# Optimization experiments

Measured on AMD Instinct MI355X. Metric: run time of the kernel, lower is better.

Reference implementation:

```python
import jax, jax.numpy as jnp
import numpy as np

N0, N1, N2, N3, B = 120000, 20000, 6000, 1600, 64
E1, E2, E3 = 480000, 144000, 38400
KS = 5  # kernel size per dim; K = 125 total


def spline_basis(pseudo, ks=KS):
    # open B-spline basis, degree 1, over [0,1]^3 (torch_spline_conv semantics)
    p = pseudo * (ks - 1)                       # (E,3)
    lo = jnp.clip(jnp.floor(p), 0.0, ks - 2.0)  # (E,3)
    f = p - lo                                  # fractional part
    bits = jnp.array([[(s >> d) & 1 for d in range(3)] for s in range(8)],
                     dtype=jnp.float32)         # (8,3) corner offsets
    w = jnp.where(bits[None] > 0, f[:, None, :], 1.0 - f[:, None, :])  # (E,8,3)
    basis = w[..., 0] * w[..., 1] * w[..., 2]   # (E,8)
    strides = jnp.array([1.0, ks, ks * ks], dtype=jnp.float32)
    kidx = ((lo[:, None, :] + bits[None]) * strides).sum(-1).astype(jnp.int32)  # (E,8)
    return basis, kidx


def spline_conv(x, edge_index, pseudo, W, root, bias, num_nodes):
    src, dst = edge_index[0], edge_index[1]
    basis, kidx = spline_basis(pseudo)                   # (E,8), (E,8)
    XW = jnp.einsum('ni,kio->nko', x, W)                 # (N,K,out)
    taps = XW[src[:, None], kidx]                        # (E,8,out) gather
    msg = (taps * basis[..., None]).sum(axis=1)          # (E,out)
    agg = jax.ops.segment_sum(msg, dst, num_segments=num_nodes)
    deg = jax.ops.segment_sum(jnp.ones_like(dst, jnp.float32), dst,
                              num_segments=num_nodes)
    agg = agg / jnp.maximum(deg, 1.0)[:, None]           # mean aggregation
    return agg + x @ root + bias


def seg_max(x, seg, n):
    v = jax.ops.segment_max(x, seg, num_segments=n)
    return jnp.where(jnp.isfinite(v), v, 0.0)  # empty voxels -> 0


def setup_inputs() -> dict:
    key = jax.random.key(0)
    ks = jax.random.split(key, 24)
    return {
        'x0': jax.random.uniform(ks[0], (N0, 1), jnp.float32),
        'cluster0': jax.random.randint(ks[1], (N0,), 0, N1),
        'edge1': jax.random.randint(ks[2], (2, E1), 0, N1),
        'pseudo1': jax.random.uniform(ks[3], (E1, 3), jnp.float32),
        'W1': jax.random.normal(ks[4], (125, 1, 64), jnp.float32) * 0.1,
        'root1': jax.random.normal(ks[5], (1, 64), jnp.float32) * 0.1,
        'b1': jnp.zeros((64,), jnp.float32),
        'cluster1': jax.random.randint(ks[6], (N1,), 0, N2),
        'edge2': jax.random.randint(ks[7], (2, E2), 0, N2),
        'pseudo2': jax.random.uniform(ks[8], (E2, 3), jnp.float32),
        'W2': jax.random.normal(ks[9], (125, 64, 64), jnp.float32) * 0.05,
        'root2': jax.random.normal(ks[10], (64, 64), jnp.float32) * 0.05,
        'b2': jnp.zeros((64,), jnp.float32),
        'cluster2': jax.random.randint(ks[11], (N2,), 0, N3),
        'edge3': jax.random.randint(ks[12], (2, E3), 0, N3),
        'pseudo3': jax.random.uniform(ks[13], (E3, 3), jnp.float32),
        'W3': jax.random.normal(ks[14], (125, 64, 128), jnp.float32) * 0.05,
        'root3': jax.random.normal(ks[15], (64, 128), jnp.float32) * 0.05,
        'b3': jnp.zeros((128,), jnp.float32),
        'cluster3': jax.random.randint(ks[16], (N3,), 0, B * 8),
        'fc1_w': jax.random.normal(ks[17], (1024, 256), jnp.float32) * 0.03,
        'fc1_b': jnp.zeros((256,), jnp.float32),
        'fc2_w': jax.random.normal(ks[18], (256, 10), jnp.float32) * 0.06,
        'fc2_b': jnp.zeros((10,), jnp.float32),
    }


def reference(x0, cluster0, edge1, pseudo1, W1, root1, b1,
              cluster1, edge2, pseudo2, W2, root2, b2,
              cluster2, edge3, pseudo3, W3, root3, b3,
              cluster3, fc1_w, fc1_b, fc2_w, fc2_b):
    x = seg_max(x0, cluster0, N1)                       # sparse voxel max pool 1
    x = jax.nn.elu(spline_conv(x, edge1, pseudo1, W1, root1, b1, N1))
    x = seg_max(x, cluster1, N2)                        # pool 2
    x = jax.nn.elu(spline_conv(x, edge2, pseudo2, W2, root2, b2, N2))
    x = seg_max(x, cluster2, N3)                        # pool 3
    x = jax.nn.elu(spline_conv(x, edge3, pseudo3, W3, root3, b3, N3))
    x = seg_max(x, cluster3, B * 8)                     # dense 2x2x2 voxel pool
    x = x.reshape(B, 8 * 128)
    x = jax.nn.elu(x @ fc1_w + fc1_b)
    x = x @ fc2_w + fc2_b
    return jax.nn.log_softmax(x, axis=1)
```

## Files before the change

### kernel.cpp

```cpp
#include <hip/hip_runtime.h>
#include <hip/hip_bf16.h>
#include <hip/hip_fp16.h>
#include <math.h>

#define N0c 120000
#define N1c 20000
#define N2c 6000
#define N3c 1600
#define E1c 480000
#define E2c 144000
#define E3c 38400

#define HB1 256
#define HB2 480
#define HB3 160
#define WCVB 125
#define SS0B  469

typedef __attribute__((ext_vector_type(8))) short short8;
typedef __attribute__((ext_vector_type(4))) float f32x4;

__device__ __forceinline__ float eluf(float x) {
    return x > 0.0f ? x : expm1f(x);
}

__device__ __forceinline__ unsigned f2sort(float f) {
    unsigned u = __float_as_uint(f);
    return (u & 0x80000000u) ? ~u : (u | 0x80000000u);
}
__device__ __forceinline__ float sort2f(unsigned u) {
    unsigned bits = (u & 0x80000000u) ? (u & 0x7FFFFFFFu) : ~u;
    return __uint_as_float(bits);
}
__device__ __forceinline__ unsigned short f2bf(float v) {
    unsigned u = __float_as_uint(v);
    unsigned r = (u + 0x7FFFu + ((u >> 16) & 1u)) >> 16;
    return (unsigned short)r;
}
__device__ __forceinline__ unsigned short f2h(float v) {
    return __half_as_ushort(__float2half(v));
}
__device__ __forceinline__ float h2f(unsigned short u) {
    return __half2float(__ushort_as_half(u));
}

__global__ __launch_bounds__(256) void hist_all(
    const int* __restrict__ edge1, const int* __restrict__ edge2,
    const int* __restrict__ edge3,
    const float* __restrict__ pseudo2, const float* __restrict__ pseudo3,
    const float* __restrict__ W2, const float* __restrict__ W3,
    const float* __restrict__ x0, const int* __restrict__ cluster0,
    int* __restrict__ blockCnt1, int* __restrict__ binTot1,
    int* __restrict__ blockCnt2, int* __restrict__ binTot2, int* __restrict__ cntD2,
    int* __restrict__ blockCnt3, int* __restrict__ binTot3, int* __restrict__ cntD3,
    unsigned short* __restrict__ W2t, unsigned short* __restrict__ W3t,
    unsigned* __restrict__ xm1)
{
    __shared__ float smf[64 * 129];
    int* h = (int*)smf;
    int b = blockIdx.x, t = threadIdx.x;
    if (b < HB1) {
        for (int i = t; i < 1250; i += 256) h[i] = 0;
        __syncthreads();
        for (int e = b * 256 + t; e < E1c; e += HB1 * 256)
            atomicAdd(&h[edge1[E1c + e] >> 4], 1);
        __syncthreads();
        for (int i = t; i < 1250; i += 256) {
            int v = h[i];
            blockCnt1[i * HB1 + b] = v;
            if (v) atomicAdd(&binTot1[i], v);
        }
    } else if (b < HB1 + HB2 + HB3) {
        bool is2 = b < HB1 + HB2;
        int rb = is2 ? (b - HB1) : (b - HB1 - HB2);
        int nblk = is2 ? HB2 : HB3;
        int E = is2 ? E2c : E3c;
        const int* edge = is2 ? edge2 : edge3;
        const float* pseudo = is2 ? pseudo2 : pseudo3;
        int* blockCnt = is2 ? blockCnt2 : blockCnt3;
        int* binTot = is2 ? binTot2 : binTot3;
        int* dstCnt = is2 ? cntD2 : cntD3;
        int nb = is2 ? HB2 : HB3;
        if (t < 64) h[t] = 0;
        __syncthreads();
        for (int e = rb * 256 + t; e < E; e += nblk * 256) {
            int c = 0, mul = 1;
            #pragma unroll
            for (int d = 0; d < 3; d++) {
                float p = pseudo[e * 3 + d] * 4.0f;
                float l = fminf(fmaxf(floorf(p), 0.0f), 3.0f);
                c += (int)l * mul;
                mul <<= 2;
            }
            atomicAdd(&h[c], 1);
            atomicAdd(&dstCnt[edge[E + e]], 1);
        }
        __syncthreads();
        if (t < 64) {
            int v = h[t];
            blockCnt[t * nb + rb] = v;
            if (v) atomicAdd(&binTot[t], v);
        }
    } else if (b < HB1 + HB2 + HB3 + WCVB) {
        int k = b - (HB1 + HB2 + HB3);
        for (int idx = t; idx < 4096; idx += 256) {
            int n = idx & 63, ic = idx >> 6;
            smf[ic * 65 + n] = W2[((size_t)k * 64 + ic) * 64 + n];
        }
        __syncthreads();
        for (int idx = t; idx < 4096; idx += 256) {
            int ic = idx & 63, n = idx >> 6;
            W2t[((size_t)k * 64 + n) * 64 + ic] = f2bf(smf[ic * 65 + n]);
        }
    } else if (b < HB1 + HB2 + HB3 + 2 * WCVB) {
        int k = b - (HB1 + HB2 + HB3 + WCVB);
        for (int idx = t; idx < 8192; idx += 256) {
            int n = idx & 127, ic = idx >> 7;
            smf[ic * 129 + n] = W3[((size_t)k * 64 + ic) * 128 + n];
        }
        __syncthreads();
        for (int idx = t; idx < 8192; idx += 256) {
            int ic = idx & 63, n = idx >> 6;
            W3t[((size_t)k * 128 + n) * 64 + ic] = f2bf(smf[ic * 129 + n]);
        }
    } else {
        int idx = (b - (HB1 + HB2 + HB3 + 2 * WCVB)) * 256 + t;
        if (idx < N0c)
            atomicMax(&xm1[cluster0[idx]], f2sort(x0[idx]));
    }
}

__global__ __launch_bounds__(256) void plan_tot(
    const int* __restrict__ binTot1, int* __restrict__ start1,
    const int* __restrict__ binTot2, int* __restrict__ binCnt2,
    int* __restrict__ binStart2, int* __restrict__ blkPrefix2,
    int* __restrict__ chunkBin2, int* __restrict__ chunkOff2,
    const int* __restrict__ binTot3, int* __restrict__ binCnt3,
    int* __restrict__ binStart3, int* __restrict__ blkPrefix3,
    int* __restrict__ chunkBin3, int* __restrict__ chunkOff3,
    const int* __restrict__ cntD2, int* __restrict__ dstStart2,
    const int* __restrict__ cntD3, int* __restrict__ dstStart3)
{
    __shared__ int ps[256];
    __shared__ int ps64[64];
    int t = threadIdx.x;

    {
        int loc[5];
        int s = 0;
        #pragma unroll
        for (int i = 0; i < 5; i++) {
            int bin = t * 5 + i;
            int v = (bin < 1250) ? binTot1[bin] : 0;
            loc[i] = v;
            s += v;
        }
        ps[t] = s;
        __syncthreads();
        for (int ofs = 1; ofs < 256; ofs <<= 1) {
            int add = (t >= ofs) ? ps[t - ofs] : 0;
            __syncthreads();
            ps[t] += add;
            __syncthreads();
        }
        int run = (t == 0) ? 0 : ps[t - 1];
        #pragma unroll
        for (int i = 0; i < 5; i++) {
            int bin = t * 5 + i;
            if (bin < 1250) {
                start1[bin] = run;
                run += loc[i];
            }
        }
        if (t == 255) start1[1250] = run;
    }
    __syncthreads();

    if (t < 64) {
        int v = binTot2[t];
        binCnt2[t] = v;
        ps64[t] = v;
    }
    __syncthreads();
    if (t == 0) {
        int s2 = 0, p = 0;
        for (int c = 0; c < 64; c++) {
            int v = ps64[c];
            binStart2[c] = s2;
            blkPrefix2[c] = p;
            s2 += v;
            p += (v + 63) >> 6;
        }
        binStart2[64] = s2;
        blkPrefix2[64] = p;
    }
    __syncthreads();
    if (t < 64) {
        int nch = (binCnt2[t] + 63) >> 6;
        int base = blkPrefix2[t];
        for (int j = 0; j < nch; j++) {
            chunkBin2[base + j] = t;
            chunkOff2[base + j] = j;
        }
    }
    __syncthreads();

    if (t < 64) {
        int v = binTot3[t];
        binCnt3[t] = v;
        ps64[t] = v;
    }
    __syncthreads();
    if (t == 0) {
        int s3 = 0, p = 0;
        for (int c = 0; c < 64; c++) {
            int v = ps64[c];
            binStart3[c] = s3;
            blkPrefix3[c] = p;
            s3 += v;
            p += (v + 63) >> 6;
        }
        binStart3[64] = s3;
        blkPrefix3[64] = p;
    }
    __syncthreads();
    if (t < 64) {
        int nch = (binCnt3[t] + 63) >> 6;
        int base = blkPrefix3[t];
        for (int j = 0; j < nch; j++) {
            chunkBin3[base + j] = t;
            chunkOff3[base + j] = j;
        }
    }
    __syncthreads();

    {
        int locd[24];
        int sd = 0;
        #pragma unroll
        for (int i = 0; i < 24; i++) {
            int bin = t * 24 + i;
            int vv = (bin < N2c) ? cntD2[bin] : 0;
            locd[i] = vv;
            sd += vv;
        }
        ps[t] = sd;
        __syncthreads();
        for (int ofs = 1; ofs < 256; ofs <<= 1) {
            int add = (t >= ofs) ? ps[t - ofs] : 0;
            __syncthreads();
            ps[t] += add;
            __syncthreads();
        }
        int rund = (t == 0) ? 0 : ps[t - 1];
        #pragma unroll
        for (int i = 0; i < 24; i++) {
            int bin = t * 24 + i;
            if (bin < N2c) { dstStart2[bin] = rund; rund += locd[i]; }
        }
        if (t == 255) dstStart2[N2c] = ps[255];
    }
    __syncthreads();

    {
        int locd[7];
        int sd = 0;
        #pragma unroll
        for (int i = 0; i < 7; i++) {
            int bin = t * 7 + i;
            int vv = (bin < N3c) ? cntD3[bin] : 0;
            locd[i] = vv;
            sd += vv;
        }
        ps[t] = sd;
        __syncthreads();
        for (int ofs = 1; ofs < 256; ofs <<= 1) {
            int add = (t >= ofs) ? ps[t - ofs] : 0;
            __syncthreads();
            ps[t] += add;
            __syncthreads();
        }
        int rund = (t == 0) ? 0 : ps[t - 1];
        #pragma unroll
        for (int i = 0; i < 7; i++) {
            int bin = t * 7 + i;
            if (bin < N3c) { dstStart3[bin] = rund; rund += locd[i]; }
        }
        if (t == 255) dstStart3[N3c] = ps[255];
    }
}

__global__ __launch_bounds__(256) void off_all(
    const int* __restrict__ blockCnt1, const int* __restrict__ start1,
    int* __restrict__ blockOff1,
    const int* __restrict__ blockCnt2, const int* __restrict__ binStart2,
    int* __restrict__ blockOff2,
    const int* __restrict__ blockCnt3, const int* __restrict__ binStart3,
    int* __restrict__ blockOff3)
{
    int wid = (blockIdx.x * 256 + threadIdx.x) >> 6;
    int lane = threadIdx.x & 63;
    if (wid >= 1250 + 64 + 64) return;
    const int* c;
    int* o;
    int run, width;
    if (wid < 1250) {
        c = blockCnt1 + (size_t)wid * HB1;
        o = blockOff1 + (size_t)wid * HB1;
        run = start1[wid];
        width = HB1;
    } else if (wid < 1250 + 64) {
        int bin = wid - 1250;
        c = blockCnt2 + (size_t)bin * HB2;
        o = blockOff2 + (size_t)bin * HB2;
        run = binStart2[bin];
        width = HB2;
    } else {
        int bin = wid - 1314;
        c = blockCnt3 + (size_t)bin * HB3;
        o = blockOff3 + (size_t)bin * HB3;
        run = binStart3[bin];
        width = HB3;
    }
    for (int base = 0; base < width; base += 64) {
        int b = base + lane;
        int v = (b < width) ? c[b] : 0;
        int inc = v;
        #pragma unroll
        for (int ofs = 1; ofs < 64; ofs <<= 1) {
            int u = __shfl_up(inc, ofs);
            if (lane >= ofs) inc += u;
        }
        if (b < width) o[b] = run + inc - v;
        run += __shfl(inc, 63);
    }
}

__global__ __launch_bounds__(256) void scatter_all(
    const int* __restrict__ edge1, const float* __restrict__ pseudo1,
    const int* __restrict__ edge2, const float* __restrict__ pseudo2,
    const int* __restrict__ edge3, const float* __restrict__ pseudo3,
    const int* __restrict__ blockOff1,
    const int* __restrict__ blockOff2, const int* __restrict__ blockOff3,
    int4* __restrict__ rec1, int4* __restrict__ rec2, int4* __restrict__ rec3,
    unsigned* __restrict__ xm1,
    const int* __restrict__ dstStart2, const int* __restrict__ dstStart3,
    int* __restrict__ curD2, int* __restrict__ curD3,
    int* __restrict__ posList2, int* __restrict__ posList3)
{
    __shared__ int cur[1250];
    int b = blockIdx.x, t = threadIdx.x;
    if (b < HB1) {
        for (int i = t; i < 1250; i += 256) cur[i] = blockOff1[(size_t)i * HB1 + b];
        __syncthreads();
        for (int e = b * 256 + t; e < E1c; e += HB1 * 256) {
            int src = edge1[e], dst = edge1[E1c + e];
            float f[3];
            int kbase = 0, mul5 = 1;
            #pragma unroll
            for (int d = 0; d < 3; d++) {
                float pp = pseudo1[e * 3 + d] * 4.0f;
                float l = fminf(fmaxf(floorf(pp), 0.0f), 3.0f);
                f[d] = pp - l;
                kbase += (int)l * mul5;
                mul5 *= 5;
            }
            int p = atomicAdd(&cur[dst >> 4], 1);
            rec1[p] = make_int4(src | ((dst & 15) << 16) | (kbase << 20),
                                __float_as_int(f[0]), __float_as_int(f[1]),
                                __float_as_int(f[2]));
        }
    } else if (b < HB1 + HB2 + HB3) {
        bool is2 = b < HB1 + HB2;
        int rb = is2 ? (b - HB1) : (b - HB1 - HB2);
        int nblk = is2 ? HB2 : HB3;
        int E = is2 ? E2c : E3c;
        const int* edge = is2 ? edge2 : edge3;
        const float* pseudo = is2 ? pseudo2 : pseudo3;
        const int* blockOff = is2 ? blockOff2 : blockOff3;
        int4* rec = is2 ? rec2 : rec3;
        const int* dstStart = is2 ? dstStart2 : dstStart3;
        int* curD = is2 ? curD2 : curD3;
        int* posList = is2 ? posList2 : posList3;
        int nb = is2 ? HB2 : HB3;
        if (t < 64) cur[t] = blockOff[(size_t)t * nb + rb];
        __syncthreads();
        for (int e = rb * 256 + t; e < E; e += nblk * 256) {
            int src = edge[e], dst = edge[E + e];
            float f[3];
            int c = 0, mul = 1;
            #pragma unroll
            for (int d = 0; d < 3; d++) {
                float pp = pseudo[e * 3 + d] * 4.0f;
                float l = fminf(fmaxf(floorf(pp), 0.0f), 3.0f);
                f[d] = pp - l;
                c += (int)l * mul;
                mul <<= 2;
            }
            int p = atomicAdd(&cur[c], 1);
            rec[p] = make_int4(src | (dst << 16),
                               __float_as_int(f[0]), __float_as_int(f[1]),
                               __float_as_int(f[2]));
            int qd = dstStart[dst] + atomicAdd(&curD[dst], 1);
            posList[qd] = p;
        }
    } else {
        int idx = (b - (HB1 + HB2 + HB3)) * 256 + t;
        if (idx < N1c) {
            float f = sort2f(xm1[idx]);
            unsigned bb = __float_as_uint(f);
            if ((bb & 0x7F800000u) == 0x7F800000u) f = 0.0f;
            ((float*)xm1)[idx] = f;
        }
    }
}

__global__ __launch_bounds__(256) void conv1_block(
    const int4* __restrict__ rec, const float* __restrict__ x,
    const int* __restrict__ start,
    const float* __restrict__ W, const float* __restrict__ root,
    const float* __restrict__ bias, const int* __restrict__ cl,
    unsigned* __restrict__ xmOut) {
    __shared__ float T[16][128];
    __shared__ float Wl[8000];
    __shared__ int degL[16];
    int b = blockIdx.x;
    int t = threadIdx.x;
    for (int j = t; j < 2048; j += 256) ((float*)T)[j] = 0.0f;
    for (int j = t; j < 8000; j += 256) Wl[j] = W[j];
    if (t < 16) degL[t] = 0;
    __syncthreads();
    int s0 = start[b], s1 = start[b + 1];
    for (int i = s0 + t; i < s1; i += 256) {
        int4 r = rec[i];
        int src = r.x & 0xFFFF;
        int ln = (r.x >> 16) & 15;
        int kbase = r.x >> 20;
        float f0 = __int_as_float(r.y);
        float f1 = __int_as_float(r.z);
        float f2 = __int_as_float(r.w);
        float xv = x[src];
        #pragma unroll
        for (int s = 0; s < 8; s++) {
            int b0 = s & 1, b1 = (s >> 1) & 1, b2 = (s >> 2) & 1;
            float w0 = b0 ? f0 : 1.0f - f0;
            float w1 = b1 ? f1 : 1.0f - f1;
            float w2 = b2 ? f2 : 1.0f - f2;
            int k = kbase + b0 + 5 * b1 + 25 * b2;
            atomicAdd(&T[ln][k], xv * w0 * w1 * w2);
        }
        atomicAdd(&degL[ln], 1);
    }
    __syncthreads();
    int w = t >> 6, lane = t & 63;
    float acc[4] = {0.0f, 0.0f, 0.0f, 0.0f};
    #pragma unroll 5
    for (int k = 0; k < 125; k++) {
        float wv = Wl[(k << 6) + lane];
        #pragma unroll
        for (int j = 0; j < 4; j++)
            acc[j] = fmaf(T[w + 4 * j][k], wv, acc[j]);
    }
    int v0 = b << 4;
    #pragma unroll
    for (int j = 0; j < 4; j++) {
        int ln = w + 4 * j;
        int v = v0 + ln;
        float d = fmaxf((float)degL[ln], 1.0f);
        float val = eluf(acc[j] / d + x[v] * root[lane] + bias[lane]);
        atomicMax(&xmOut[((size_t)cl[v] << 6) + lane], f2sort(val));
    }
}

__global__ void decode_cvt(unsigned* __restrict__ buf,
                           unsigned short* __restrict__ xb, int total) {
    int idx = blockIdx.x * blockDim.x + threadIdx.x;
    if (idx >= total) return;
    float f = sort2f(buf[idx]);
    unsigned b = __float_as_uint(f);
    if ((b & 0x7F800000u) == 0x7F800000u) f = 0.0f;
    ((float*)buf)[idx] = f;
    xb[idx] = f2bf(f);
}

template<int COUT>
__global__ __launch_bounds__(256) void spline_mfma(
    const int4* __restrict__ recs,
    const unsigned short* __restrict__ Wt,
    const unsigned short* __restrict__ xb,
    const int* __restrict__ binStart,
    const int* __restrict__ binCnt,
    const int* __restrict__ blkPrefix,
    const int* __restrict__ chunkBin,
    const int* __restrict__ chunkOff,
    unsigned short* __restrict__ msg)
{
    __shared__ float basisS[4][8][64];
    __shared__ int srcS[4][64];

    int w = threadIdx.x >> 6, lane = threadIdx.x & 63;
    int c = blockIdx.x * 4 + w;
    if (c >= blkPrefix[64]) return;
    int bin = chunkBin[c];
    int chunk = chunkOff[c];
    int cnt = binCnt[bin];

    {
        int pos = chunk * 64 + lane;
        bool act = pos < cnt;
        int4 r = act ? recs[binStart[bin] + pos] : make_int4(0, 0, 0, 0);
        srcS[w][lane] = r.x & 0xFFFF;
        float f0 = __int_as_float(r.y);
        float f1 = __int_as_float(r.z);
        float f2 = __int_as_float(r.w);
        #pragma unroll
        for (int s = 0; s < 8; s++) {
            float w0 = (s & 1) ? f0 : 1.0f - f0;
            float w1 = (s & 2) ? f1 : 1.0f - f1;
            float w2 = (s & 4) ? f2 : 1.0f - f2;
            basisS[w][s][lane] = act ? (w0 * w1 * w2) : 0.0f;
        }
    }
    __builtin_amdgcn_wave_barrier();
    __threadfence_block();

    int lo0 = bin & 3, lo1 = (bin >> 2) & 3, lo2 = bin >> 4;
    int kbase = lo0 + 5 * lo1 + 25 * lo2;
    int colOff = (COUT == 128) ? (blockIdx.y << 6) : 0;
    int q = lane >> 4;
    int mcol = lane & 15;

    short8 afr[4][2];
    #pragma unroll
    for (int rt = 0; rt < 4; rt++) {
        int src = srcS[w][rt * 16 + mcol];
        const unsigned short* xr = xb + ((size_t)src << 6) + q * 8;
        afr[rt][0] = *(const short8*)(xr);
        afr[rt][1] = *(const short8*)(xr + 32);
    }

    f32x4 acc[4][4];
    #pragma unroll
    for (int rt = 0; rt < 4; rt++)
        #pragma unroll
        for (int nt = 0; nt < 4; nt++)
            acc[rt][nt] = (f32x4){0.0f, 0.0f, 0.0f, 0.0f};
    const f32x4 zero4 = {0.0f, 0.0f, 0.0f, 0.0f};

    #pragma unroll 1
    for (int s = 0; s < 8; s++) {
        int k = kbase + (s & 1) + 5 * ((s >> 1) & 1) + 25 * (s >> 2);
        const unsigned short* Wk = Wt + ((size_t)k * COUT + colOff) * 64;
        short8 bfr[4][2];
        #pragma unroll
        for (int nt = 0; nt < 4; nt++) {
            const unsigned short* Wn = Wk + (size_t)(nt * 16 + mcol) * 64 + q * 8;
            bfr[nt][0] = *(const short8*)(Wn);
            bfr[nt][1] = *(const short8*)(Wn + 32);
        }
        #pragma unroll
        for (int rt = 0; rt < 4; rt++) {
            f32x4 ct[4];
            #pragma unroll
            for (int nt = 0; nt < 4; nt++) {
                ct[nt] = __builtin_amdgcn_mfma_f32_16x16x32_bf16(afr[rt][0], bfr[nt][0], zero4, 0, 0, 0);
                ct[nt] = __builtin_amdgcn_mfma_f32_16x16x32_bf16(afr[rt][1], bfr[nt][1], ct[nt], 0, 0, 0);
            }
            #pragma unroll
            for (int r = 0; r < 4; r++) {
                float bs = basisS[w][s][rt * 16 + q * 4 + r];
                #pragma unroll
                for (int nt = 0; nt < 4; nt++)
                    acc[rt][nt][r] = fmaf(bs, ct[nt][r], acc[rt][nt][r]);
            }
        }
    }

    int base = binStart[bin] + chunk * 64;
    #pragma unroll
    for (int rt = 0; rt < 4; rt++) {
        #pragma unroll
        for (int r = 0; r < 4; r++) {
            int row = rt * 16 + q * 4 + r;
            if (chunk * 64 + row < cnt) {
                unsigned short* mp = msg + (size_t)(base + row) * COUT + colOff + mcol;
                #pragma unroll
                for (int nt = 0; nt < 4; nt++)
                    mp[nt * 16] = f2h(acc[rt][nt][r]);
            }
        }
    }
}

__global__ __launch_bounds__(256) void agg_update64(
    const unsigned short* __restrict__ msg, const int* __restrict__ posList,
    const int* __restrict__ dstStart,
    const float* __restrict__ xm, const float* __restrict__ root,
    const float* __restrict__ bias, const int* __restrict__ cl,
    unsigned* __restrict__ xmOut, int nNodes) {
    __shared__ float xsh[4][64];
    int w = threadIdx.x >> 6, lane = threadIdx.x & 63;
    int v = blockIdx.x * 4 + w;
    if (v >= nNodes) return;
    xsh[w][lane] = xm[((size_t)v << 6) + lane];
    int s0 = dstStart[v], s1 = dstStart[v + 1];
    float a0 = 0.0f, a1 = 0.0f, a2 = 0.0f, a3 = 0.0f;
    int i = s0;
    for (; i + 4 <= s1; i += 4) {
        int p0 = posList[i], p1 = posList[i + 1];
        int p2 = posList[i + 2], p3 = posList[i + 3];
        a0 += h2f(msg[((size_t)p0 << 6) + lane]);
        a1 += h2f(msg[((size_t)p1 << 6) + lane]);
        a2 += h2f(msg[((size_t)p2 << 6) + lane]);
        a3 += h2f(msg[((size_t)p3 << 6) + lane]);
    }
    for (; i < s1; i++)
        a0 += h2f(msg[((size_t)posList[i] << 6) + lane]);
    float a = (a0 + a1 + a2 + a3) / fmaxf((float)(s1 - s0), 1.0f);
    float r = 0.0f;
    #pragma unroll 8
    for (int j = 0; j < 64; j++)
        r = fmaf(xsh[w][j], root[(j << 6) + lane], r);
    float val = eluf(a + r + bias[lane]);
    atomicMax(&xmOut[((size_t)cl[v] << 6) + lane], f2sort(val));
}

__global__ __launch_bounds__(256) void agg_update128(
    const unsigned short* __restrict__ msg, const int* __restrict__ posList,
    const int* __restrict__ dstStart,
    const float* __restrict__ xm, const float* __restrict__ root,
    const float* __restrict__ bias, const int* __restrict__ cl,
    unsigned* __restrict__ xmOut, int nNodes) {
    __shared__ float xsh[4][64];
    int w = threadIdx.x >> 6, lane = threadIdx.x & 63;
    int v = blockIdx.x * 4 + w;
    if (v >= nNodes) return;
    xsh[w][lane] = xm[((size_t)v << 6) + lane];
    int s0 = dstStart[v], s1 = dstStart[v + 1];
    float c0a = 0.0f, c0b = 0.0f, c1a = 0.0f, c1b = 0.0f;
    int i = s0;
    for (; i + 2 <= s1; i += 2) {
        int p0 = posList[i], p1 = posList[i + 1];
        const unsigned short* m0 = msg + ((size_t)p0 << 7);
        const unsigned short* m1 = msg + ((size_t)p1 << 7);
        c0a += h2f(m0[lane]); c0b += h2f(m0[64 + lane]);
        c1a += h2f(m1[lane]); c1b += h2f(m1[64 + lane]);
    }
    for (; i < s1; i++) {
        const unsigned short* m0 = msg + ((size_t)posList[i] << 7);
        c0a += h2f(m0[lane]); c0b += h2f(m0[64 + lane]);
    }
    float dinv = 1.0f / fmaxf((float)(s1 - s0), 1.0f);
    float aa0 = (c0a + c1a) * dinv;
    float aa1 = (c0b + c1b) * dinv;
    float r0 = 0.0f, r1 = 0.0f;
    #pragma unroll 8
    for (int j = 0; j < 64; j++) {
        float xi = xsh[w][j];
        r0 = fmaf(xi, root[(j << 7) + lane], r0);
        r1 = fmaf(xi, root[(j << 7) + 64 + lane], r1);
    }
    unsigned* orow = xmOut + ((size_t)cl[v] << 7);
    atomicMax(&orow[lane], f2sort(eluf(aa0 + r0 + bias[lane])));
    atomicMax(&orow[64 + lane], f2sort(eluf(aa1 + r1 + bias[lane + 64])));
}

__global__ __launch_bounds__(256) void fc1_split(
    const unsigned* __restrict__ xin, const float* __restrict__ w1,
    float* __restrict__ h) {
    __shared__ float xsh[128];
    int row = blockIdx.x, ks = blockIdx.y;
    int o = threadIdx.x;
    if (o < 128) {
        float f = sort2f(xin[row * 1024 + ks * 128 + o]);
        unsigned bb = __float_as_uint(f);
        if ((bb & 0x7F800000u) == 0x7F800000u) f = 0.0f;
        xsh[o] = f;
    }
    __syncthreads();
    float acc = 0.0f;
    const float* wp = w1 + (size_t)ks * 128 * 256 + o;
    #pragma unroll 8
    for (int i = 0; i < 128; i++)
        acc = fmaf(xsh[i], wp[i * 256], acc);
    atomicAdd(&h[row * 256 + o], acc);
}

__global__ __launch_bounds__(64) void fc2_k(
    const float* __restrict__ h, const float* __restrict__ b1,
    const float* __restrict__ w2, const float* __restrict__ b2,
    float* __restrict__ out) {
    __shared__ float hs[256];
    __shared__ float lg[10];
    int row = blockIdx.x;
    int t = threadIdx.x;
    for (int i = t; i < 256; i += 64) hs[i] = eluf(h[row * 256 + i] + b1[i]);
    __syncthreads();
    if (t < 10) {
        float a = b2[t];
        for (int i = 0; i < 256; i++) a = fmaf(hs[i], w2[i * 10 + t], a);
        lg[t] = a;
    }
    __syncthreads();
    if (t < 10) {
        float m = -1e30f;
        #pragma unroll
        for (int j = 0; j < 10; j++) m = fmaxf(m, lg[j]);
        float sum = 0.0f;
        #pragma unroll
        for (int j = 0; j < 10; j++) sum += expf(lg[j] - m);
        out[row * 10 + t] = lg[t] - m - logf(sum);
    }
}

extern "C" void kernel_launch(void* const* d_in, const int* in_sizes, int n_in,
                              void* d_out, int out_size, void* d_ws, size_t ws_size,
                              hipStream_t stream) {
    const float* x0      = (const float*)d_in[0];
    const int*   cluster0= (const int*)d_in[1];
    const int*   edge1   = (const int*)d_in[2];
    const float* pseudo1 = (const float*)d_in[3];
    const float* W1      = (const float*)d_in[4];
    const float* root1   = (const float*)d_in[5];
    const float* b1      = (const float*)d_in[6];
    const int*   cluster1= (const int*)d_in[7];
    const int*   edge2   = (const int*)d_in[8];
    const float* pseudo2 = (const float*)d_in[9];
    const float* W2      = (const float*)d_in[10];
    const float* root2   = (const float*)d_in[11];
    const float* b2      = (const float*)d_in[12];
    const int*   cluster2= (const int*)d_in[13];
    const int*   edge3   = (const int*)d_in[14];
    const float* pseudo3 = (const float*)d_in[15];
    const float* W3      = (const float*)d_in[16];
    const float* root3   = (const float*)d_in[17];
    const float* b3      = (const float*)d_in[18];
    const int*   cluster3= (const int*)d_in[19];
    const float* fc1_w   = (const float*)d_in[20];
    const float* fc1_b   = (const float*)d_in[21];
    const float* fc2_w   = (const float*)d_in[22];
    const float* fc2_b   = (const float*)d_in[23];
    float* out = (float*)d_out;

    float* ws = (float*)d_ws;
    size_t off = 0;
    float* xm1  = ws + off; off += 20480;
    float* xm2  = ws + off; off += (size_t)N2c * 64;
    float* xm3  = ws + off; off += (size_t)N3c * 64;
    float* xm4  = ws + off; off += 512 * 128;
    float* h1   = ws + off; off += 64 * 256;
    int* cntD2   = (int*)(ws + off); off += 6016;
    int* cntD3   = (int*)(ws + off); off += 1664;
    int* curD2   = (int*)(ws + off); off += 6016;
    int* curD3   = (int*)(ws + off); off += 1664;
    int* binTot1 = (int*)(ws + off); off += 1280;
    int* binTot2 = (int*)(ws + off); off += 64;
    int* binTot3 = (int*)(ws + off); off += 64;
    size_t zeroFloats = off;
    int4* rec1 = (int4*)(ws + off); off += (size_t)E1c * 4;
    int4* rec2 = (int4*)(ws + off); off += (size_t)E2c * 4;
    int4* rec3 = (int4*)(ws + off); off += (size_t)E3c * 4;
    unsigned short* W2t = (unsigned short*)(ws + off); off += 256000;
    unsigned short* W3t = (unsigned short*)(ws + off); off += 512000;
    unsigned short* xb2 = (unsigned short*)(ws + off); off += 192000;
    unsigned short* xb3 = (unsigned short*)(ws + off); off += 51200;
    int* start1    = (int*)(ws + off); off += 1280;
    int* blockCnt1 = (int*)(ws + off); off += (size_t)HB1 * 1250;
    int* blockOff1 = (int*)(ws + off); off += (size_t)HB1 * 1250;
    int* blockCnt2 = (int*)(ws + off); off += (size_t)HB2 * 64;
    int* blockOff2 = (int*)(ws + off); off += (size_t)HB2 * 64;
    int* blockCnt3 = (int*)(ws + off); off += (size_t)HB3 * 64;
    int* blockOff3 = (int*)(ws + off); off += (size_t)HB3 * 64;
    int* binCnt2   = (int*)(ws + off); off += 64;
    int* binStart2 = (int*)(ws + off); off += 80;
    int* blkPrefix2= (int*)(ws + off); off += 80;
    int* chunkBin2 = (int*)(ws + off); off += 2560;
    int* chunkOff2 = (int*)(ws + off); off += 2560;
    int* binCnt3   = (int*)(ws + off); off += 64;
    int* binStart3 = (int*)(ws + off); off += 80;
    int* blkPrefix3= (int*)(ws + off); off += 80;
    int* chunkBin3 = (int*)(ws + off); off += 768;
    int* chunkOff3 = (int*)(ws + off); off += 768;
    int* dstStart2 = (int*)(ws + off); off += 6016;
    int* dstStart3 = (int*)(ws + off); off += 1664;
    int* posList2  = (int*)(ws + off); off += E2c;
    int* posList3  = (int*)(ws + off); off += E3c;
    unsigned short* msg = (unsigned short*)(ws + off); off += (size_t)E2c * 32;

    hipMemsetAsync(d_ws, 0, zeroFloats * sizeof(float), stream);

    hist_all<<<HB1 + HB2 + HB3 + 2 * WCVB + SS0B, 256, 0, stream>>>(
        edge1, edge2, edge3, pseudo2, pseudo3, W2, W3, x0, cluster0,
        blockCnt1, binTot1, blockCnt2, binTot2, cntD2,
        blockCnt3, binTot3, cntD3, W2t, W3t, (unsigned*)xm1);

    plan_tot<<<1, 256, 0, stream>>>(
        binTot1, start1,
        binTot2, binCnt2, binStart2, blkPrefix2, chunkBin2, chunkOff2,
        binTot3, binCnt3, binStart3, blkPrefix3, chunkBin3, chunkOff3,
        cntD2, dstStart2, cntD3, dstStart3);

    off_all<<<(1378 * 64 + 255) / 256, 256, 0, stream>>>(
        blockCnt1, start1, blockOff1,
        blockCnt2, binStart2, blockOff2,
        blockCnt3, binStart3, blockOff3);

    scatter_all<<<HB1 + HB2 + HB3 + (N1c + 255) / 256, 256, 0, stream>>>(
        edge1, pseudo1, edge2, pseudo2, edge3, pseudo3,
        blockOff1, blockOff2, blockOff3, rec1, rec2, rec3, (unsigned*)xm1,
        dstStart2, dstStart3, curD2, curD3, posList2, posList3);

    conv1_block<<<1250, 256, 0, stream>>>(rec1, xm1, start1, W1, root1, b1,
                                          cluster1, (unsigned*)xm2);
    decode_cvt<<<(N2c * 64) / 256, 256, 0, stream>>>((unsigned*)xm2, xb2, N2c * 64);

    spline_mfma<64><<<dim3((E2c / 64 + 64 + 3) / 4, 1), 256, 0, stream>>>(
        rec2, W2t, xb2, binStart2, binCnt2, blkPrefix2, chunkBin2, chunkOff2, msg);
    agg_update64<<<(N2c + 3) / 4, 256, 0, stream>>>(msg, posList2, dstStart2,
                                                    xm2, root2, b2, cluster2,
                                                    (unsigned*)xm3, N2c);
    decode_cvt<<<(N3c * 64) / 256, 256, 0, stream>>>((unsigned*)xm3, xb3, N3c * 64);

    spline_mfma<128><<<dim3((E3c / 64 + 64 + 3) / 4, 2), 256, 0, stream>>>(
        rec3, W3t, xb3, binStart3, binCnt3, blkPrefix3, chunkBin3, chunkOff3, msg);
    agg_update128<<<(N3c + 3) / 4, 256, 0, stream>>>(msg, posList3, dstStart3,
                                                     xm3, root3, b3, cluster3,
                                                     (unsigned*)xm4, N3c);

    fc1_split<<<dim3(64, 8), 256, 0, stream>>>((unsigned*)xm4, fc1_w, h1);
    fc2_k<<<64, 64, 0, stream>>>(h1, fc1_b, fc2_w, fc2_b, out);
}
```

Baseline: 325.4 us.

## Pre-gather conv1 source features into records and drop shared weight staging

The xm1 decode pass moves from scatter_all into off_all so that xm1 is finished before scattering. scatter_all can then read x1[src] once per edge and pack it into the record, with f0 stored as half precision. This removes the random gather of x inside conv1_block. conv1_block also stops copying the 8000-float W1 into shared memory and reads W directly from global memory, which lowers LDS use and may raise occupancy, at the cost of global or cache reads in the 125-step inner loop and some precision lost on f0.

```diff
diff --git a/kernel.cpp b/kernel.cpp
--- a/kernel.cpp
+++ b/kernel.cpp
@@ -16,6 +16,8 @@
 #define HB3 160
 #define WCVB 125
 #define SS0B  469
+#define OFFB  345
+#define DECB  79
 
 typedef __attribute__((ext_vector_type(8))) short short8;
 typedef __attribute__((ext_vector_type(4))) float f32x4;
@@ -296,8 +298,19 @@
     const int* __restrict__ blockCnt2, const int* __restrict__ binStart2,
     int* __restrict__ blockOff2,
     const int* __restrict__ blockCnt3, const int* __restrict__ binStart3,
-    int* __restrict__ blockOff3)
+    int* __restrict__ blockOff3,
+    unsigned* __restrict__ xm1)
 {
+    if (blockIdx.x >= OFFB) {
+        int idx = (blockIdx.x - OFFB) * 256 + threadIdx.x;
+        if (idx < N1c) {
+            float f = sort2f(xm1[idx]);
+            unsigned bb = __float_as_uint(f);
+            if ((bb & 0x7F800000u) == 0x7F800000u) f = 0.0f;
+            ((float*)xm1)[idx] = f;
+        }
+        return;
+    }
     int wid = (blockIdx.x * 256 + threadIdx.x) >> 6;
     int lane = threadIdx.x & 63;
     if (wid >= 1250 + 64 + 64) return;
@@ -343,7 +356,7 @@
     const int* __restrict__ blockOff1,
     const int* __restrict__ blockOff2, const int* __restrict__ blockOff3,
     int4* __restrict__ rec1, int4* __restrict__ rec2, int4* __restrict__ rec3,
-    unsigned* __restrict__ xm1,
+    const float* __restrict__ x1,
     const int* __restrict__ dstStart2, const int* __restrict__ dstStart3,
     int* __restrict__ curD2, int* __restrict__ curD3,
     int* __restrict__ posList2, int* __restrict__ posList3)
@@ -365,12 +378,13 @@
                 kbase += (int)l * mul5;
                 mul5 *= 5;
             }
+            float xv = x1[src];
             int p = atomicAdd(&cur[dst >> 4], 1);
-            rec1[p] = make_int4(src | ((dst & 15) << 16) | (kbase << 20),
-                                __float_as_int(f[0]), __float_as_int(f[1]),
+            rec1[p] = make_int4(((int)f2h(f[0]) << 16) | (kbase << 4) | (dst & 15),
+                                __float_as_int(xv), __float_as_int(f[1]),
                                 __float_as_int(f[2]));
         }
-    } else if (b < HB1 + HB2 + HB3) {
+    } else {
         bool is2 = b < HB1 + HB2;
         int rb = is2 ? (b - HB1) : (b - HB1 - HB2);
         int nblk = is2 ? HB2 : HB3;
@@ -404,14 +418,6 @@
             int qd = dstStart[dst] + atomicAdd(&curD[dst], 1);
             posList[qd] = p;
         }
-    } else {
-        int idx = (b - (HB1 + HB2 + HB3)) * 256 + t;
-        if (idx < N1c) {
-            float f = sort2f(xm1[idx]);
-            unsigned bb = __float_as_uint(f);
-            if ((bb & 0x7F800000u) == 0x7F800000u) f = 0.0f;
-            ((float*)xm1)[idx] = f;
-        }
     }
 }
 
@@ -422,24 +428,21 @@
     const float* __restrict__ bias, const int* __restrict__ cl,
     unsigned* __restrict__ xmOut) {
     __shared__ float T[16][128];
-    __shared__ float Wl[8000];
     __shared__ int degL[16];
     int b = blockIdx.x;
     int t = threadIdx.x;
     for (int j = t; j < 2048; j += 256) ((float*)T)[j] = 0.0f;
-    for (int j = t; j < 8000; j += 256) Wl[j] = W[j];
     if (t < 16) degL[t] = 0;
     __syncthreads();
     int s0 = start[b], s1 = start[b + 1];
     for (int i = s0 + t; i < s1; i += 256) {
         int4 r = rec[i];
-        int src = r.x & 0xFFFF;
-        int ln = (r.x >> 16) & 15;
-        int kbase = r.x >> 20;
-        float f0 = __int_as_float(r.y);
+        int ln = r.x & 15;
+        int kbase = (r.x >> 4) & 127;
+        float f0 = h2f((unsigned short)((unsigned)r.x >> 16));
+        float xv = __int_as_float(r.y);
         float f1 = __int_as_float(r.z);
         float f2 = __int_as_float(r.w);
-        float xv = x[src];
         #pragma unroll
         for (int s = 0; s < 8; s++) {
             int b0 = s & 1, b1 = (s >> 1) & 1, b2 = (s >> 2) & 1;
@@ -454,9 +457,8 @@
     __syncthreads();
     int w = t >> 6, lane = t & 63;
     float acc[4] = {0.0f, 0.0f, 0.0f, 0.0f};
-    #pragma unroll 5
     for (int k = 0; k < 125; k++) {
-        float wv = Wl[(k << 6) + lane];
+        float wv = W[(k << 6) + lane];
         #pragma unroll
         for (int j = 0; j < 4; j++)
             acc[j] = fmaf(T[w + 4 * j][k], wv, acc[j]);
@@ -800,14 +802,14 @@
         binTot3, binCnt3, binStart3, blkPrefix3, chunkBin3, chunkOff3,
         cntD2, dstStart2, cntD3, dstStart3);
 
-    off_all<<<(1378 * 64 + 255) / 256, 256, 0, stream>>>(
+    off_all<<<OFFB + DECB, 256, 0, stream>>>(
         blockCnt1, start1, blockOff1,
         blockCnt2, binStart2, blockOff2,
-        blockCnt3, binStart3, blockOff3);
-
-    scatter_all<<<HB1 + HB2 + HB3 + (N1c + 255) / 256, 256, 0, stream>>>(
+        blockCnt3, binStart3, blockOff3, (unsigned*)xm1);
+
+    scatter_all<<<HB1 + HB2 + HB3, 256, 0, stream>>>(
         edge1, pseudo1, edge2, pseudo2, edge3, pseudo3,
-        blockOff1, blockOff2, blockOff3, rec1, rec2, rec3, (unsigned*)xm1,
+        blockOff1, blockOff2, blockOff3, rec1, rec2, rec3, xm1,
         dstStart2, dstStart3, curD2, curD3, posList2, posList3);
 
     conv1_block<<<1250, 256, 0, stream>>>(rec1, xm1, start1, W1, root1, b1,
```

New measurement: 322.9 us. Within noise of the previous version (-0.8%).
